# Optimization experiments

Measured on AMD Instinct MI355X. Metric: run time of the kernel, lower is better.

The kernel has to match this reference:

```python
import jax, jax.numpy as jnp
import numpy as np

SEQ, BATCH, IN, HID = 2048, 128, 128, 256
ALPHA = 0.1  # dt/tau = 10/100


def setup_inputs() -> dict:
    key = jax.random.key(0)
    ks = jax.random.split(key, 5)
    x = jax.random.normal(ks[0], (SEQ, BATCH, IN), dtype=jnp.float32)
    h0 = jnp.zeros((BATCH, HID), dtype=jnp.float32)
    W_in = jax.random.normal(ks[1], (HID, IN), dtype=jnp.float32) / np.sqrt(IN)
    b_in = jax.random.normal(ks[2], (HID,), dtype=jnp.float32) * 0.01
    W_h = jax.random.normal(ks[3], (HID, HID), dtype=jnp.float32) / np.sqrt(HID)
    b_h = jax.random.normal(ks[4], (HID,), dtype=jnp.float32) * 0.01
    return {"x": x, "h0": h0, "W_in": W_in, "b_in": b_in, "W_h": W_h, "b_h": b_h}


def reference(x, h0, W_in, b_in, W_h, b_h):
    # Precompute input projection for all timesteps in one GEMM: (S,B,H)
    xin = jnp.einsum('sbi,hi->sbh', x, W_in) + b_in

    def step(h, xin_t):
        h_new = jax.nn.relu(xin_t + h @ W_h.T + b_h)
        h = h * (1.0 - ALPHA) + h_new * ALPHA
        return h, h

    h_final, outputs = jax.lax.scan(step, h0, xin)
    return outputs, h_final
```

## Files before the change

### kernel.cpp

```cpp
#include <hip/hip_runtime.h>

#define SEQ   2048
#define BATCH 128
#define INDIM 128
#define HID   256
#define BH    (BATCH * HID)
#define SB    (SEQ * BATCH)

template <int CTRL>
__device__ __forceinline__ float dpp_mov_f32(float v) {
  return __int_as_float(
      __builtin_amdgcn_update_dpp(0, __float_as_int(v), CTRL, 0xF, 0xF, false));
}
__device__ __forceinline__ float sum8(float v) {
  v += dpp_mov_f32<0xB1>(v);
  v += dpp_mov_f32<0x4E>(v);
  v += dpp_mov_f32<0x141>(v);
  return v;
}

#define P1_ROWS 64

__global__ __launch_bounds__(128, 1) void xin_gemm(
    const float* __restrict__ x, const float* __restrict__ W_in,
    const float* __restrict__ b_in, const float* __restrict__ b_h,
    float* __restrict__ out) {
  __shared__ __align__(16) float xs[P1_ROWS * INDIM];
  const int j2 = threadIdx.x;
  const int r0 = blockIdx.x * P1_ROWS;

  float w0[INDIM], w1[INDIM];
  {
    const float4* wg0 = (const float4*)(W_in + (size_t)j2 * INDIM);
    const float4* wg1 = (const float4*)(W_in + (size_t)(j2 + 128) * INDIM);
#pragma unroll
    for (int k4 = 0; k4 < INDIM / 4; ++k4) {
      float4 v0 = wg0[k4], v1 = wg1[k4];
      w0[4*k4+0] = v0.x; w0[4*k4+1] = v0.y; w0[4*k4+2] = v0.z; w0[4*k4+3] = v0.w;
      w1[4*k4+0] = v1.x; w1[4*k4+1] = v1.y; w1[4*k4+2] = v1.z; w1[4*k4+3] = v1.w;
    }
  }

  {
    const float4* xg = (const float4*)(x + (size_t)r0 * INDIM);
    float4* xs4 = (float4*)xs;
#pragma unroll
    for (int q = 0; q < (P1_ROWS * INDIM / 4) / 128; ++q)
      xs4[q * 128 + j2] = xg[q * 128 + j2];
  }
  __syncthreads();

  const float bias0 = b_in[j2] + b_h[j2];
  const float bias1 = b_in[j2 + 128] + b_h[j2 + 128];

  for (int rr = 0; rr < P1_ROWS; rr += 4) {
    float a0 = bias0, a1 = bias0, a2 = bias0, a3 = bias0;
    float c0 = bias1, c1 = bias1, c2 = bias1, c3 = bias1;
    const float4* x0 = (const float4*)(xs + (size_t)(rr + 0) * INDIM);
    const float4* x1 = (const float4*)(xs + (size_t)(rr + 1) * INDIM);
    const float4* x2 = (const float4*)(xs + (size_t)(rr + 2) * INDIM);
    const float4* x3 = (const float4*)(xs + (size_t)(rr + 3) * INDIM);
#pragma unroll
    for (int k4 = 0; k4 < INDIM / 4; ++k4) {
      float4 v0 = x0[k4], v1 = x1[k4], v2 = x2[k4], v3 = x3[k4];
      a0 = fmaf(w0[4*k4+0], v0.x, a0); a0 = fmaf(w0[4*k4+1], v0.y, a0);
      a0 = fmaf(w0[4*k4+2], v0.z, a0); a0 = fmaf(w0[4*k4+3], v0.w, a0);
      a1 = fmaf(w0[4*k4+0], v1.x, a1); a1 = fmaf(w0[4*k4+1], v1.y, a1);
      a1 = fmaf(w0[4*k4+2], v1.z, a1); a1 = fmaf(w0[4*k4+3], v1.w, a1);
      a2 = fmaf(w0[4*k4+0], v2.x, a2); a2 = fmaf(w0[4*k4+1], v2.y, a2);
      a2 = fmaf(w0[4*k4+2], v2.z, a2); a2 = fmaf(w0[4*k4+3], v2.w, a2);
      a3 = fmaf(w0[4*k4+0], v3.x, a3); a3 = fmaf(w0[4*k4+1], v3.y, a3);
      a3 = fmaf(w0[4*k4+2], v3.z, a3); a3 = fmaf(w0[4*k4+3], v3.w, a3);
      c0 = fmaf(w1[4*k4+0], v0.x, c0); c0 = fmaf(w1[4*k4+1], v0.y, c0);
      c0 = fmaf(w1[4*k4+2], v0.z, c0); c0 = fmaf(w1[4*k4+3], v0.w, c0);
      c1 = fmaf(w1[4*k4+0], v1.x, c1); c1 = fmaf(w1[4*k4+1], v1.y, c1);
      c1 = fmaf(w1[4*k4+2], v1.z, c1); c1 = fmaf(w1[4*k4+3], v1.w, c1);
      c2 = fmaf(w1[4*k4+0], v2.x, c2); c2 = fmaf(w1[4*k4+1], v2.y, c2);
      c2 = fmaf(w1[4*k4+2], v2.z, c2); c2 = fmaf(w1[4*k4+3], v2.w, c2);
      c3 = fmaf(w1[4*k4+0], v3.x, c3); c3 = fmaf(w1[4*k4+1], v3.y, c3);
      c3 = fmaf(w1[4*k4+2], v3.z, c3); c3 = fmaf(w1[4*k4+3], v3.w, c3);
    }
    out[(size_t)(r0 + rr + 0) * HID + j2] = a0;
    out[(size_t)(r0 + rr + 1) * HID + j2] = a1;
    out[(size_t)(r0 + rr + 2) * HID + j2] = a2;
    out[(size_t)(r0 + rr + 3) * HID + j2] = a3;
    out[(size_t)(r0 + rr + 0) * HID + j2 + 128] = c0;
    out[(size_t)(r0 + rr + 1) * HID + j2 + 128] = c1;
    out[(size_t)(r0 + rr + 2) * HID + j2 + 128] = c2;
    out[(size_t)(r0 + rr + 3) * HID + j2 + 128] = c3;
  }
}

#define PADS 36

__global__ __launch_bounds__(512, 2) void ctrnn_rec(
    const float* __restrict__ h0, const float* __restrict__ W_h,
    float* out) {
  __shared__ __align__(16) float hs[2][8 * PADS];

  const int b   = blockIdx.x;
  const int tid = threadIdx.x;
  const int q   = tid & 7;
  const int g   = tid >> 3;

  float w[4][32];
#pragma unroll
  for (int i = 0; i < 4; ++i) {
    const float4* wg = (const float4*)(W_h + (size_t)(4 * g + i) * HID + 32 * q);
#pragma unroll
    for (int k4 = 0; k4 < 8; ++k4) {
      float4 v = wg[k4];
      w[i][4*k4+0] = v.x; w[i][4*k4+1] = v.y;
      w[i][4*k4+2] = v.z; w[i][4*k4+3] = v.w;
    }
  }

  float4 h4 = *(const float4*)(h0 + (size_t)b * HID + 4 * g);
  float hr[4] = {h4.x, h4.y, h4.z, h4.w};

  float* const wslot0 = &hs[0][PADS * (g >> 3) + 4 * (g & 7)];
  float* const wslot1 = &hs[1][PADS * (g >> 3) + 4 * (g & 7)];
  const float* const rbase0 = &hs[0][PADS * q];
  const float* const rbase1 = &hs[1][PADS * q];

  if (q == 0) *(float4*)wslot0 = h4;

  float* const io = out + (size_t)b * HID + 4 * g;
  float4 xA = *(const float4*)(io);
  float4 xB = *(const float4*)(io + (size_t)BH);

  __syncthreads();

  auto step = [&](int t, const float* rbuf, float* wslot) {
    float4 xC = xA;
    if (t + 2 < SEQ) xC = *(const float4*)(io + (size_t)(t + 2) * BH);

    const float4* hv = (const float4*)rbuf;
    float a[4] = {0.f, 0.f, 0.f, 0.f};
#pragma unroll
    for (int k4 = 0; k4 < 8; ++k4) {
      float4 v = hv[k4];
#pragma unroll
      for (int i = 0; i < 4; ++i) {
        a[i] = fmaf(w[i][4*k4+0], v.x, a[i]);
        a[i] = fmaf(w[i][4*k4+1], v.y, a[i]);
        a[i] = fmaf(w[i][4*k4+2], v.z, a[i]);
        a[i] = fmaf(w[i][4*k4+3], v.w, a[i]);
      }
    }
#pragma unroll
    for (int i = 0; i < 4; ++i) a[i] = sum8(a[i]);

    const float xi[4] = {xA.x, xA.y, xA.z, xA.w};
#pragma unroll
    for (int i = 0; i < 4; ++i)
      hr[i] = fmaf(0.1f, fmaxf(a[i] + xi[i], 0.f), 0.9f * hr[i]);

    if (q == 0) {
      float4 hw = make_float4(hr[0], hr[1], hr[2], hr[3]);
      *(float4*)wslot = hw;
      *(float4*)(io + (size_t)t * BH) = hw;
    }
    xA = xB; xB = xC;
    __syncthreads();
  };

  for (int t = 0; t < SEQ; t += 2) {
    step(t, rbase0, wslot1);
    step(t + 1, rbase1, wslot0);
  }

  if (q == 0)
    *(float4*)(io + (size_t)SEQ * BH) = make_float4(hr[0], hr[1], hr[2], hr[3]);
}

extern "C" void kernel_launch(void* const* d_in, const int* in_sizes, int n_in,
                              void* d_out, int out_size, void* d_ws, size_t ws_size,
                              hipStream_t stream) {
  const float* x    = (const float*)d_in[0];
  const float* h0   = (const float*)d_in[1];
  const float* W_in = (const float*)d_in[2];
  const float* b_in = (const float*)d_in[3];
  const float* W_h  = (const float*)d_in[4];
  const float* b_h  = (const float*)d_in[5];
  float* out = (float*)d_out;

  xin_gemm<<<SB / P1_ROWS, 128, 0, stream>>>(x, W_in, b_in, b_h, out);
  ctrnn_rec<<<BATCH, 512, 0, stream>>>(h0, W_h, out);
}
```

Baseline: 2.840 ms.

## Retile input GEMM with LDS tiles and halve recurrence block to 256 threads

```diff
diff --git a/kernel.cpp b/kernel.cpp
--- a/kernel.cpp
+++ b/kernel.cpp
@@ -19,81 +19,88 @@
   return v;
 }
 
-#define P1_ROWS 64
-
-__global__ __launch_bounds__(128, 1) void xin_gemm(
+#define TM 128
+#define TN 128
+#define KC 64
+
+__global__ __launch_bounds__(256, 2) void xin_gemm(
     const float* __restrict__ x, const float* __restrict__ W_in,
     const float* __restrict__ b_in, const float* __restrict__ b_h,
     float* __restrict__ out) {
-  __shared__ __align__(16) float xs[P1_ROWS * INDIM];
-  const int j2 = threadIdx.x;
-  const int r0 = blockIdx.x * P1_ROWS;
-
-  float w0[INDIM], w1[INDIM];
-  {
-    const float4* wg0 = (const float4*)(W_in + (size_t)j2 * INDIM);
-    const float4* wg1 = (const float4*)(W_in + (size_t)(j2 + 128) * INDIM);
-#pragma unroll
-    for (int k4 = 0; k4 < INDIM / 4; ++k4) {
-      float4 v0 = wg0[k4], v1 = wg1[k4];
-      w0[4*k4+0] = v0.x; w0[4*k4+1] = v0.y; w0[4*k4+2] = v0.z; w0[4*k4+3] = v0.w;
-      w1[4*k4+0] = v1.x; w1[4*k4+1] = v1.y; w1[4*k4+2] = v1.z; w1[4*k4+3] = v1.w;
-    }
-  }
-
-  {
-    const float4* xg = (const float4*)(x + (size_t)r0 * INDIM);
-    float4* xs4 = (float4*)xs;
-#pragma unroll
-    for (int q = 0; q < (P1_ROWS * INDIM / 4) / 128; ++q)
-      xs4[q * 128 + j2] = xg[q * 128 + j2];
-  }
-  __syncthreads();
-
-  const float bias0 = b_in[j2] + b_h[j2];
-  const float bias1 = b_in[j2 + 128] + b_h[j2 + 128];
-
-  for (int rr = 0; rr < P1_ROWS; rr += 4) {
-    float a0 = bias0, a1 = bias0, a2 = bias0, a3 = bias0;
-    float c0 = bias1, c1 = bias1, c2 = bias1, c3 = bias1;
-    const float4* x0 = (const float4*)(xs + (size_t)(rr + 0) * INDIM);
-    const float4* x1 = (const float4*)(xs + (size_t)(rr + 1) * INDIM);
-    const float4* x2 = (const float4*)(xs + (size_t)(rr + 2) * INDIM);
-    const float4* x3 = (const float4*)(xs + (size_t)(rr + 3) * INDIM);
-#pragma unroll
-    for (int k4 = 0; k4 < INDIM / 4; ++k4) {
-      float4 v0 = x0[k4], v1 = x1[k4], v2 = x2[k4], v3 = x3[k4];
-      a0 = fmaf(w0[4*k4+0], v0.x, a0); a0 = fmaf(w0[4*k4+1], v0.y, a0);
-      a0 = fmaf(w0[4*k4+2], v0.z, a0); a0 = fmaf(w0[4*k4+3], v0.w, a0);
-      a1 = fmaf(w0[4*k4+0], v1.x, a1); a1 = fmaf(w0[4*k4+1], v1.y, a1);
-      a1 = fmaf(w0[4*k4+2], v1.z, a1); a1 = fmaf(w0[4*k4+3], v1.w, a1);
-      a2 = fmaf(w0[4*k4+0], v2.x, a2); a2 = fmaf(w0[4*k4+1], v2.y, a2);
-      a2 = fmaf(w0[4*k4+2], v2.z, a2); a2 = fmaf(w0[4*k4+3], v2.w, a2);
-      a3 = fmaf(w0[4*k4+0], v3.x, a3); a3 = fmaf(w0[4*k4+1], v3.y, a3);
-      a3 = fmaf(w0[4*k4+2], v3.z, a3); a3 = fmaf(w0[4*k4+3], v3.w, a3);
-      c0 = fmaf(w1[4*k4+0], v0.x, c0); c0 = fmaf(w1[4*k4+1], v0.y, c0);
-      c0 = fmaf(w1[4*k4+2], v0.z, c0); c0 = fmaf(w1[4*k4+3], v0.w, c0);
-      c1 = fmaf(w1[4*k4+0], v1.x, c1); c1 = fmaf(w1[4*k4+1], v1.y, c1);
-      c1 = fmaf(w1[4*k4+2], v1.z, c1); c1 = fmaf(w1[4*k4+3], v1.w, c1);
-      c2 = fmaf(w1[4*k4+0], v2.x, c2); c2 = fmaf(w1[4*k4+1], v2.y, c2);
-      c2 = fmaf(w1[4*k4+2], v2.z, c2); c2 = fmaf(w1[4*k4+3], v2.w, c2);
-      c3 = fmaf(w1[4*k4+0], v3.x, c3); c3 = fmaf(w1[4*k4+1], v3.y, c3);
-      c3 = fmaf(w1[4*k4+2], v3.z, c3); c3 = fmaf(w1[4*k4+3], v3.w, c3);
-    }
-    out[(size_t)(r0 + rr + 0) * HID + j2] = a0;
-    out[(size_t)(r0 + rr + 1) * HID + j2] = a1;
-    out[(size_t)(r0 + rr + 2) * HID + j2] = a2;
-    out[(size_t)(r0 + rr + 3) * HID + j2] = a3;
-    out[(size_t)(r0 + rr + 0) * HID + j2 + 128] = c0;
-    out[(size_t)(r0 + rr + 1) * HID + j2 + 128] = c1;
-    out[(size_t)(r0 + rr + 2) * HID + j2 + 128] = c2;
-    out[(size_t)(r0 + rr + 3) * HID + j2 + 128] = c3;
+  __shared__ __align__(16) float As[TM * KC];
+  __shared__ __align__(16) float Bs[TN * KC];
+
+  const int tid = threadIdx.x;
+  const int bm  = blockIdx.x >> 1;
+  const int bn  = blockIdx.x & 1;
+  const int mg  = tid & 15;
+  const int ng  = tid >> 4;
+  const int rotA = 4 * (mg & 7);
+  const int rotB = 4 * (ng & 7);
+
+  const float4* xg = (const float4*)(x + (size_t)bm * TM * INDIM);
+  const float4* wg = (const float4*)(W_in + (size_t)bn * TN * INDIM);
+
+  float acc[8][8] = {};
+
+  for (int h = 0; h < 2; ++h) {
+#pragma unroll
+    for (int s = 0; s < 8; ++s) {
+      const int id = tid + 256 * s;
+      const int r  = id >> 4;
+      const int c4 = id & 15;
+      const int rc = (4 * c4 + 4 * ((r >> 3) & 7)) & (KC - 1);
+      float4 va = xg[(size_t)r * 32 + c4 + 16 * h];
+      *(float4*)(As + r * KC + rc) = va;
+      float4 vb = wg[(size_t)r * 32 + c4 + 16 * h];
+      *(float4*)(Bs + r * KC + rc) = vb;
+    }
+    __syncthreads();
+
+#pragma unroll 4
+    for (int k4 = 0; k4 < KC / 4; ++k4) {
+      const int ca = (4 * k4 + rotA) & (KC - 1);
+      const int cb = (4 * k4 + rotB) & (KC - 1);
+      float4 a[8], bb[8];
+#pragma unroll
+      for (int i = 0; i < 8; ++i)
+        a[i] = *(const float4*)(As + (8 * mg + i) * KC + ca);
+#pragma unroll
+      for (int j = 0; j < 8; ++j)
+        bb[j] = *(const float4*)(Bs + (8 * ng + j) * KC + cb);
+#pragma unroll
+      for (int i = 0; i < 8; ++i)
+#pragma unroll
+        for (int j = 0; j < 8; ++j) {
+          acc[i][j] = fmaf(a[i].x, bb[j].x, acc[i][j]);
+          acc[i][j] = fmaf(a[i].y, bb[j].y, acc[i][j]);
+          acc[i][j] = fmaf(a[i].z, bb[j].z, acc[i][j]);
+          acc[i][j] = fmaf(a[i].w, bb[j].w, acc[i][j]);
+        }
+    }
+    __syncthreads();
+  }
+
+  const int row0 = bm * TM + 8 * mg;
+  const int n0   = bn * TN + 8 * ng;
+  float bi[8];
+#pragma unroll
+  for (int j = 0; j < 8; ++j) bi[j] = b_in[n0 + j] + b_h[n0 + j];
+#pragma unroll
+  for (int i = 0; i < 8; ++i) {
+    float4 lo = make_float4(acc[i][0] + bi[0], acc[i][1] + bi[1],
+                            acc[i][2] + bi[2], acc[i][3] + bi[3]);
+    float4 hi = make_float4(acc[i][4] + bi[4], acc[i][5] + bi[5],
+                            acc[i][6] + bi[6], acc[i][7] + bi[7]);
+    float* o = out + (size_t)(row0 + i) * HID + n0;
+    *(float4*)o       = lo;
+    *(float4*)(o + 4) = hi;
   }
 }
 
 #define PADS 36
 
-__global__ __launch_bounds__(512, 2) void ctrnn_rec(
+__global__ __launch_bounds__(256, 1) void ctrnn_rec(
     const float* __restrict__ h0, const float* __restrict__ W_h,
     float* out) {
   __shared__ __align__(16) float hs[2][8 * PADS];
@@ -103,10 +110,10 @@
   const int q   = tid & 7;
   const int g   = tid >> 3;
 
-  float w[4][32];
-#pragma unroll
-  for (int i = 0; i < 4; ++i) {
-    const float4* wg = (const float4*)(W_h + (size_t)(4 * g + i) * HID + 32 * q);
+  float w[8][32];
+#pragma unroll
+  for (int i = 0; i < 8; ++i) {
+    const float4* wg = (const float4*)(W_h + (size_t)(8 * g + i) * HID + 32 * q);
 #pragma unroll
     for (int k4 = 0; k4 < 8; ++k4) {
       float4 v = wg[k4];
@@ -115,33 +122,46 @@
     }
   }
 
-  float4 h4 = *(const float4*)(h0 + (size_t)b * HID + 4 * g);
-  float hr[4] = {h4.x, h4.y, h4.z, h4.w};
-
-  float* const wslot0 = &hs[0][PADS * (g >> 3) + 4 * (g & 7)];
-  float* const wslot1 = &hs[1][PADS * (g >> 3) + 4 * (g & 7)];
-  const float* const rbase0 = &hs[0][PADS * q];
-  const float* const rbase1 = &hs[1][PADS * q];
-
-  if (q == 0) *(float4*)wslot0 = h4;
-
-  float* const io = out + (size_t)b * HID + 4 * g;
-  float4 xA = *(const float4*)(io);
-  float4 xB = *(const float4*)(io + (size_t)BH);
+  float hr[8];
+  {
+    float4 h40 = *(const float4*)(h0 + (size_t)b * HID + 8 * g);
+    float4 h41 = *(const float4*)(h0 + (size_t)b * HID + 8 * g + 4);
+    hr[0]=h40.x; hr[1]=h40.y; hr[2]=h40.z; hr[3]=h40.w;
+    hr[4]=h41.x; hr[5]=h41.y; hr[6]=h41.z; hr[7]=h41.w;
+  }
+
+  float* const wslot0 = &hs[0][PADS * (g >> 2) + 8 * (g & 3)];
+  float* const wslot1 = &hs[1][PADS * (g >> 2) + 8 * (g & 3)];
+  const float* const rb0 = &hs[0][PADS * q];
+  const float* const rb1 = &hs[1][PADS * q];
+
+  if (q == 0) {
+    *(float4*)wslot0       = make_float4(hr[0], hr[1], hr[2], hr[3]);
+    *(float4*)(wslot0 + 4) = make_float4(hr[4], hr[5], hr[6], hr[7]);
+  }
+
+  float* const io = out + (size_t)b * HID + 8 * g;
+  float4 xA0 = ((const float4*)io)[0];
+  float4 xA1 = ((const float4*)io)[1];
+  float4 xB0 = ((const float4*)(io + (size_t)BH))[0];
+  float4 xB1 = ((const float4*)(io + (size_t)BH))[1];
 
   __syncthreads();
 
   auto step = [&](int t, const float* rbuf, float* wslot) {
-    float4 xC = xA;
-    if (t + 2 < SEQ) xC = *(const float4*)(io + (size_t)(t + 2) * BH);
+    float4 xC0 = xA0, xC1 = xA1;
+    if (t + 2 < SEQ) {
+      xC0 = ((const float4*)(io + (size_t)(t + 2) * BH))[0];
+      xC1 = ((const float4*)(io + (size_t)(t + 2) * BH))[1];
+    }
 
     const float4* hv = (const float4*)rbuf;
-    float a[4] = {0.f, 0.f, 0.f, 0.f};
+    float a[8] = {0.f, 0.f, 0.f, 0.f, 0.f, 0.f, 0.f, 0.f};
 #pragma unroll
     for (int k4 = 0; k4 < 8; ++k4) {
       float4 v = hv[k4];
 #pragma unroll
-      for (int i = 0; i < 4; ++i) {
+      for (int i = 0; i < 8; ++i) {
         a[i] = fmaf(w[i][4*k4+0], v.x, a[i]);
         a[i] = fmaf(w[i][4*k4+1], v.y, a[i]);
         a[i] = fmaf(w[i][4*k4+2], v.z, a[i]);
@@ -149,29 +169,37 @@
       }
     }
 #pragma unroll
-    for (int i = 0; i < 4; ++i) a[i] = sum8(a[i]);
-
-    const float xi[4] = {xA.x, xA.y, xA.z, xA.w};
-#pragma unroll
-    for (int i = 0; i < 4; ++i)
+    for (int i = 0; i < 8; ++i) a[i] = sum8(a[i]);
+
+    const float xi[8] = {xA0.x, xA0.y, xA0.z, xA0.w,
+                         xA1.x, xA1.y, xA1.z, xA1.w};
+#pragma unroll
+    for (int i = 0; i < 8; ++i)
       hr[i] = fmaf(0.1f, fmaxf(a[i] + xi[i], 0.f), 0.9f * hr[i]);
 
     if (q == 0) {
-      float4 hw = make_float4(hr[0], hr[1], hr[2], hr[3]);
-      *(float4*)wslot = hw;
-      *(float4*)(io + (size_t)t * BH) = hw;
-    }
-    xA = xB; xB = xC;
+      float4 lo = make_float4(hr[0], hr[1], hr[2], hr[3]);
+      float4 hi = make_float4(hr[4], hr[5], hr[6], hr[7]);
+      *(float4*)wslot       = lo;
+      *(float4*)(wslot + 4) = hi;
+      float* o = io + (size_t)t * BH;
+      *(float4*)o       = lo;
+      *(float4*)(o + 4) = hi;
+    }
+    xA0 = xB0; xA1 = xB1; xB0 = xC0; xB1 = xC1;
     __syncthreads();
   };
 
   for (int t = 0; t < SEQ; t += 2) {
-    step(t, rbase0, wslot1);
-    step(t + 1, rbase1, wslot0);
-  }
-
-  if (q == 0)
-    *(float4*)(io + (size_t)SEQ * BH) = make_float4(hr[0], hr[1], hr[2], hr[3]);
+    step(t, rb0, wslot1);
+    step(t + 1, rb1, wslot0);
+  }
+
+  if (q == 0) {
+    float* o = io + (size_t)SEQ * BH;
+    *(float4*)o       = make_float4(hr[0], hr[1], hr[2], hr[3]);
+    *(float4*)(o + 4) = make_float4(hr[4], hr[5], hr[6], hr[7]);
+  }
 }
 
 extern "C" void kernel_launch(void* const* d_in, const int* in_sizes, int n_in,
@@ -185,6 +213,6 @@
   const float* b_h  = (const float*)d_in[5];
   float* out = (float*)d_out;
 
-  xin_gemm<<<SB / P1_ROWS, 128, 0, stream>>>(x, W_in, b_in, b_h, out);
-  ctrnn_rec<<<BATCH, 512, 0, stream>>>(h0, W_h, out);
-}
+  xin_gemm<<<(SB / TM) * (HID / TN), 256, 0, stream>>>(x, W_in, b_in, b_h, out);
+  ctrnn_rec<<<BATCH, 256, 0, stream>>>(h0, W_h, out);
+}
```

New measurement: 2.839 ms. No clear change (-0.0%).
